# Kernel optimization log

Measured on AMD Instinct MI355X. Metric: run time of the kernel, lower is better.

Reference implementation:

```python
import jax, jax.numpy as jnp
import numpy as np

T, B, IN = 1000, 16, 440
H0, H1 = 512, 512


def setup_inputs() -> dict:
    key = jax.random.key(0)
    ks = iter(jax.random.split(key, 64))

    def w(shape, s=0.02):
        return jax.random.normal(next(ks), shape, jnp.float32) * s

    inp = {"x": jax.random.normal(next(ks), (T, B, IN), jnp.float32)}
    # layer 0 consumes IN features; layer 1 consumes 2*H0 (bidir concat)
    for li, (din, h) in enumerate([(IN, H0), (2 * H0, H1)]):
        for g in "fioc":
            inp[f"W{g}{li}"] = w((h, din))          # x-gate Linear weight
            inp[f"b{g}{li}"] = jnp.zeros((h,), jnp.float32)  # x-gate bias
            inp[f"U{g}{li}"] = w((h, h))            # recurrent Linear (no bias)
    return inp


def _lstm_layer(x, Wf, bf, Wi, bi, Wo, bo, Wc, bc, Uf, Ui, Uo, Uc):
    # Precompute input-to-gate projections for all timesteps (as the torch code does).
    gf = jnp.einsum('tbi,hi->tbh', x, Wf) + bf
    gi = jnp.einsum('tbi,hi->tbh', x, Wi) + bi
    go = jnp.einsum('tbi,hi->tbh', x, Wo) + bo
    gc = jnp.einsum('tbi,hi->tbh', x, Wc) + bc
    B2, H = x.shape[1], Wf.shape[0]

    def step(carry, g):
        ht, ct = carry
        gft, git, got, gct = g
        ft = jax.nn.sigmoid(gft + ht @ Uf.T)
        it = jax.nn.sigmoid(git + ht @ Ui.T)
        ot = jax.nn.sigmoid(got + ht @ Uo.T)
        # drop_mask == 1.0 in eval mode (lstm_drop = 0.0)
        ct = it * jnp.tanh(gct + ht @ Uc.T) + ft * ct
        ht = ot * jnp.tanh(ct)
        return (ht, ct), ht

    init = (jnp.zeros((B2, H), x.dtype), jnp.zeros((B2, H), x.dtype))
    _, h = jax.lax.scan(step, init, (gf, gi, go, gc))
    return h  # [T, B2, H]


def _bidir_layer(x, params):
    Bb = x.shape[1]
    # bidir: concat forward stream with time-flipped stream along batch dim
    x2 = jnp.concatenate([x, x[::-1]], axis=1)
    h = _lstm_layer(x2, *params)
    h_f = h[:, :Bb]
    h_b = h[:, Bb:][::-1]  # flip backward stream back to forward time
    return jnp.concatenate([h_f, h_b], axis=2)


def reference(x,
              Wf0, bf0, Uf0, Wi0, bi0, Ui0, Wo0, bo0, Uo0, Wc0, bc0, Uc0,
              Wf1, bf1, Uf1, Wi1, bi1, Ui1, Wo1, bo1, Uo1, Wc1, bc1, Uc1):
    p0 = (Wf0, bf0, Wi0, bi0, Wo0, bo0, Wc0, bc0, Uf0, Ui0, Uo0, Uc0)
    p1 = (Wf1, bf1, Wi1, bi1, Wo1, bo1, Wc1, bc1, Uf1, Ui1, Uo1, Uc1)
    h = _bidir_layer(x, p0)
    h = _bidir_layer(h, p1)
    return h  # [T, B, 2*H1]
```

## Files before the change

### kernel.cpp

```cpp
#include <hip/hip_runtime.h>
#include <hip/hip_bf16.h>
#include <stdint.h>


typedef __attribute__((ext_vector_type(8))) short bf16x8;
typedef __attribute__((ext_vector_type(4))) float f32x4;
typedef __attribute__((ext_vector_type(4))) int i32x4;

__device__ __forceinline__ unsigned short f2bf(float f) {
    union { float f; unsigned int u; } v; v.f = f;
    unsigned int u = v.u;
    return (unsigned short)((u + 0x7fffu + ((u >> 16) & 1u)) >> 16);
}
__device__ __forceinline__ float bf2f(unsigned short b) {
    union { unsigned int u; float f; } v; v.u = ((unsigned int)b) << 16;
    return v.f;
}
__device__ __forceinline__ float fsig(float x) { return 1.f / (1.f + __expf(-x)); }
__device__ __forceinline__ float ftanh(float x) { return 1.f - 2.f / (1.f + __expf(2.f * x)); }


__device__ __forceinline__ unsigned int coh_ld32(const void* p) {
    unsigned int v;
    asm volatile("global_load_dword %0, %1, off sc0 sc1\n\ts_waitcnt vmcnt(0)"
                 : "=v"(v) : "v"(p) : "memory");
    return v;
}
__device__ __forceinline__ void coh_ld128_issue(i32x4& d, const void* p) {
    asm volatile("global_load_dwordx4 %0, %1, off sc0 sc1" : "=&v"(d) : "v"(p) : "memory");
}
__device__ __forceinline__ void coh_st32(void* p, unsigned int v) {
    asm volatile("global_store_dword %0, %1, off sc0 sc1" :: "v"(p), "v"(v) : "memory");
}
__device__ __forceinline__ void vm_drain() {
    asm volatile("s_waitcnt vmcnt(0)" ::: "memory");
}


__global__ void pack_x_kernel(const float* __restrict__ x, unsigned short* __restrict__ xp,
                              int M, int K, int Kp) {
    int total = M * Kp;
    for (int idx = blockIdx.x * blockDim.x + threadIdx.x; idx < total;
         idx += gridDim.x * blockDim.x) {
        int r = idx / Kp, k = idx - r * Kp;
        xp[idx] = (k < K) ? f2bf(x[(size_t)r * K + k]) : (unsigned short)0;
    }
}

__global__ void pack_w_kernel(const float* __restrict__ Wf, const float* __restrict__ Wi,
                              const float* __restrict__ Wo, const float* __restrict__ Wc,
                              unsigned short* __restrict__ out, int K, int Kp) {
    int total = 2048 * Kp;
    for (int idx = blockIdx.x * blockDim.x + threadIdx.x; idx < total;
         idx += gridDim.x * blockDim.x) {
        int n = idx / Kp, k = idx - n * Kp;
        int gate = n >> 9, j = n & 511;
        const float* W = (gate == 0) ? Wf : (gate == 1) ? Wi : (gate == 2) ? Wo : Wc;
        out[idx] = (k < K) ? f2bf(W[(size_t)j * K + k]) : (unsigned short)0;
    }
}


__global__ __launch_bounds__(256) void gemm_gates(
    const unsigned short* __restrict__ A, const unsigned short* __restrict__ Bm,
    const float* __restrict__ bF, const float* __restrict__ bI,
    const float* __restrict__ bO, const float* __restrict__ bC,
    unsigned short* __restrict__ G, int Kp) {
    __shared__ unsigned short Alds[64][32];
    __shared__ unsigned short Blds[64][32];
    const int tid = threadIdx.x;
    const int m0 = blockIdx.x * 64;
    const int n0 = blockIdx.y * 64;
    const int w = tid >> 6, l = tid & 63;
    const int lr = l & 15, lk = (l >> 4) * 8;
    const int ldrow = tid >> 2;
    const int ldk = (tid & 3) * 8;
    const unsigned short* Aptr = A + (size_t)(m0 + ldrow) * Kp + ldk;
    const unsigned short* Bptr = Bm + (size_t)(n0 + ldrow) * Kp + ldk;

    f32x4 zero = {0.f, 0.f, 0.f, 0.f};
    f32x4 acc0 = zero, acc1 = zero, acc2 = zero, acc3 = zero;

    for (int k0 = 0; k0 < Kp; k0 += 32) {
        *(uint4*)&Alds[ldrow][ldk] = *(const uint4*)(Aptr + k0);
        *(uint4*)&Blds[ldrow][ldk] = *(const uint4*)(Bptr + k0);
        __syncthreads();
        bf16x8 a = *(const bf16x8*)&Alds[w * 16 + lr][lk];
        bf16x8 b0 = *(const bf16x8*)&Blds[0 * 16 + lr][lk];
        bf16x8 b1 = *(const bf16x8*)&Blds[1 * 16 + lr][lk];
        bf16x8 b2 = *(const bf16x8*)&Blds[2 * 16 + lr][lk];
        bf16x8 b3 = *(const bf16x8*)&Blds[3 * 16 + lr][lk];
        acc0 = __builtin_amdgcn_mfma_f32_16x16x32_bf16(a, b0, acc0, 0, 0, 0);
        acc1 = __builtin_amdgcn_mfma_f32_16x16x32_bf16(a, b1, acc1, 0, 0, 0);
        acc2 = __builtin_amdgcn_mfma_f32_16x16x32_bf16(a, b2, acc2, 0, 0, 0);
        acc3 = __builtin_amdgcn_mfma_f32_16x16x32_bf16(a, b3, acc3, 0, 0, 0);
        __syncthreads();
    }
    const int gate = n0 >> 9;
    const float* bias = (gate == 0) ? bF : (gate == 1) ? bI : (gate == 2) ? bO : bC;
    f32x4 accs[4] = {acc0, acc1, acc2, acc3};
#pragma unroll
    for (int c = 0; c < 4; ++c) {
        int col = n0 + c * 16 + lr;
        float bv = bias[col & 511];
#pragma unroll
        for (int r = 0; r < 4; ++r) {
            int row = m0 + w * 16 + (l >> 4) * 4 + r;
            G[(size_t)row * 2048 + col] = f2bf(accs[c][r] + bv);
        }
    }
}


template <int LAYER>
__global__ __launch_bounds__(256, 1) void lstm_rec4(
    const unsigned short* __restrict__ U, const unsigned short* __restrict__ G,
    unsigned short* __restrict__ y_bf, float* __restrict__ y_f32,
    unsigned short* __restrict__ h_frag, unsigned int* __restrict__ flags, int T) {
    __shared__ unsigned short wlds[4 * 16 * 64 * 8];

    const int tid = threadIdx.x;
    const int w = tid >> 6;
    const int l = tid & 63;
    const int wg = blockIdx.x;
    const int j0 = wg * 16;
    const int g = l & 3;
    const int q = (l & 15) >> 2;
    const int jl = 4 * w + q;
    const int m0 = (l >> 4) * 4 + g;
    const int mrow = (l >> 4) * 4;
    const int colg = g * 512 + j0 + jl;
    const int kcw = wg >> 1;
    const int jlq = ((wg & 1) << 4) + jl;
    const int lslot = m0 + 16 * (jlq >> 3);
    const int jb = jlq & 7;

    for (int e = tid; e < 4096; e += 256) {
        int fl = e >> 6;
        int ll = e & 63;
        int nt = fl >> 4, kc = fl & 15;
        int nl = nt * 16 + (ll & 15);
        int jj = nl >> 2, gg = nl & 3;
        int nglob = gg * 512 + j0 + jj;
        int k = kc * 32 + (ll >> 4) * 8;
        *(uint4*)&wlds[(size_t)e * 8] = *(const uint4*)&U[(size_t)nglob * 512 + k];
    }

    {
        unsigned int* h0w = (unsigned int*)h_frag;
        coh_st32(&h0w[wg * 256 + tid], 0u);
        vm_drain();
        __syncthreads();
        if (tid == 0) coh_st32(&flags[wg * 32], 1u);
    }

    unsigned short gpf[2][4];
    {
        const unsigned short* gf_ = G + (size_t)mrow * 2048 + colg;
        const unsigned short* gb_ = G + (size_t)((T - 1) * 16 + mrow) * 2048 + colg;
#pragma unroll
        for (int r = 0; r < 4; ++r) {
            gpf[0][r] = gf_[r * 2048];
            gpf[1][r] = gb_[r * 2048];
        }
    }

    float cst[2][4] = {{0.f, 0.f, 0.f, 0.f}, {0.f, 0.f, 0.f, 0.f}};

    for (int s = 0; s < T; ++s) {
        unsigned short gcur[2][4];
#pragma unroll
        for (int r = 0; r < 4; ++r) {
            gcur[0][r] = gpf[0][r];
            gcur[1][r] = gpf[1][r];
        }
        {
            int sn = (s + 1 < T) ? (s + 1) : (T - 1);
            const unsigned short* gf_ = G + (size_t)(sn * 16 + mrow) * 2048 + colg;
            const unsigned short* gb_ = G + (size_t)((T - 1 - sn) * 16 + mrow) * 2048 + colg;
#pragma unroll
            for (int r = 0; r < 4; ++r) {
                gpf[0][r] = gf_[r * 2048];
                gpf[1][r] = gb_[r * 2048];
            }
        }

        if (w == 0) {
            unsigned tgt = (unsigned)(s + 1);
            int guard = 0;
            while (true) {
                unsigned u = 0xFFFFFFFFu;
                if (l < 32) u = coh_ld32(&flags[l * 32]);
                if (__all(u >= tgt) || ++guard > (1 << 14)) break;
            }
        }
        __syncthreads();

        const unsigned short* hb = h_frag + (size_t)(s & 1) * 16384;
        i32x4 ha0[16], ha1[16];
#pragma unroll
        for (int kc = 0; kc < 16; ++kc) {
            coh_ld128_issue(ha0[kc], hb + ((size_t)(0 * 16 + kc) * 64 + l) * 8);
            coh_ld128_issue(ha1[kc], hb + ((size_t)(1 * 16 + kc) * 64 + l) * 8);
        }
        vm_drain();
        __builtin_amdgcn_sched_barrier(0);

        f32x4 acc0 = {0.f, 0.f, 0.f, 0.f};
        f32x4 acc1 = {0.f, 0.f, 0.f, 0.f};
#pragma unroll
        for (int kc = 0; kc < 16; ++kc) {
            union { i32x4 i; bf16x8 v; } c0, c1;
            c0.i = ha0[kc];
            c1.i = ha1[kc];
            bf16x8 bw = *(const bf16x8*)&wlds[(((size_t)w * 16 + kc) * 64 + l) * 8];
            acc0 = __builtin_amdgcn_mfma_f32_16x16x32_bf16(c0.v, bw, acc0, 0, 0, 0);
            acc1 = __builtin_amdgcn_mfma_f32_16x16x32_bf16(c1.v, bw, acc1, 0, 0, 0);
        }

        float hsel[2];
#pragma unroll
        for (int mb = 0; mb < 2; ++mb) {
            f32x4 acc = mb ? acc1 : acc0;
#pragma unroll
            for (int r = 0; r < 4; ++r) {
                float v = acc[r] + bf2f(gcur[mb][r]);
                float x1 = __shfl_xor(v, 1, 64);
                float x2 = __shfl_xor(v, 2, 64);
                float x3 = __shfl_xor(x1, 2, 64);
                bool b0 = (g & 1) != 0, b1 = (g & 2) != 0;
                float gf = b1 ? (b0 ? x3 : x2) : (b0 ? x1 : v);
                float gi = b1 ? (b0 ? x2 : x3) : (b0 ? v : x1);
                float go = b1 ? (b0 ? x1 : v) : (b0 ? x3 : x2);
                float gc = b1 ? (b0 ? v : x1) : (b0 ? x2 : x3);
                float ft = fsig(gf), it = fsig(gi), ot = fsig(go);
                float cn = it * ftanh(gc) + ft * cst[mb][r];
                cst[mb][r] = cn;
                float hn = ot * ftanh(cn);
                if (r == g) hsel[mb] = hn;
            }
        }

        const int p1 = (s + 1) & 1;
        unsigned hw0, hw1;
        float ho0, ho1;
        {
            unsigned b16 = (unsigned)f2bf(hsel[0]);
            unsigned ho = (unsigned)__shfl_xor((int)b16, 4, 64);
            hw0 = b16 | (ho << 16);
            ho0 = __shfl_xor(hsel[0], 4, 64);
            b16 = (unsigned)f2bf(hsel[1]);
            ho = (unsigned)__shfl_xor((int)b16, 4, 64);
            hw1 = b16 | (ho << 16);
            ho1 = __shfl_xor(hsel[1], 4, 64);
        }
        if ((q & 1) == 0) {
#pragma unroll
            for (int mb = 0; mb < 2; ++mb) {
                unsigned word = mb ? hw1 : hw0;
                size_t base =
                    (size_t)p1 * 16384 + ((size_t)(mb * 16 + kcw) * 64 + lslot) * 8 + jb;
                coh_st32(h_frag + base, word);
                int row = (mb ? (T - 1 - s) : s) * 16 + m0;
                int col = mb * 512 + j0 + jl;
                if (LAYER == 0) {
                    *(unsigned int*)&y_bf[(size_t)row * 1024 + col] = word;
                } else {
                    float2 fv = make_float2(hsel[mb], mb ? ho1 : ho0);
                    *(float2*)&y_f32[(size_t)row * 1024 + col] = fv;
                }
            }
        }

        vm_drain();
        __syncthreads();
        if (tid == 0) coh_st32(&flags[wg * 32], (unsigned)(s + 2));
    }
}


extern "C" void kernel_launch(void* const* d_in, const int* in_sizes, int n_in,
                              void* d_out, int out_size, void* d_ws, size_t ws_size,
                              hipStream_t stream) {
    (void)in_sizes; (void)n_in; (void)out_size; (void)ws_size;
    const int T = 1000, M = T * 16;
    const int K0 = 440, K0p = 448, K1 = 1024;

    char* ws = (char*)d_ws;
    size_t off = 0;
    auto alloc = [&](size_t bytes) -> void* {
        void* p = ws + off;
        off += (bytes + 255) & ~(size_t)255;
        return p;
    };
    unsigned short* G  = (unsigned short*)alloc((size_t)M * 2048 * 2);
    unsigned short* xp = (unsigned short*)alloc((size_t)M * K0p * 2);
    unsigned short* W0 = (unsigned short*)alloc((size_t)2048 * K0p * 2);
    unsigned short* W1 = (unsigned short*)alloc((size_t)2048 * K1 * 2);
    unsigned short* U0 = (unsigned short*)alloc((size_t)2048 * 512 * 2);
    unsigned short* U1 = (unsigned short*)alloc((size_t)2048 * 512 * 2);
    unsigned short* y0 = (unsigned short*)alloc((size_t)M * 1024 * 2);
    unsigned short* hf = (unsigned short*)alloc((size_t)2 * 16384 * 2);
    unsigned int* fl0  = (unsigned int*)alloc((size_t)32 * 32 * 4);
    unsigned int* fl1  = (unsigned int*)alloc((size_t)32 * 32 * 4);

    const float* x = (const float*)d_in[0];

    hipMemsetAsync(fl0, 0, 32 * 32 * 4, stream);
    hipMemsetAsync(fl1, 0, 32 * 32 * 4, stream);

    pack_x_kernel<<<2048, 256, 0, stream>>>(x, xp, M, K0, K0p);
    pack_w_kernel<<<1024, 256, 0, stream>>>((const float*)d_in[1], (const float*)d_in[4],
                                            (const float*)d_in[7], (const float*)d_in[10],
                                            W0, K0, K0p);
    pack_w_kernel<<<1024, 256, 0, stream>>>((const float*)d_in[3], (const float*)d_in[6],
                                            (const float*)d_in[9], (const float*)d_in[12],
                                            U0, 512, 512);
    pack_w_kernel<<<1024, 256, 0, stream>>>((const float*)d_in[13], (const float*)d_in[16],
                                            (const float*)d_in[19], (const float*)d_in[22],
                                            W1, K1, K1);
    pack_w_kernel<<<1024, 256, 0, stream>>>((const float*)d_in[15], (const float*)d_in[18],
                                            (const float*)d_in[21], (const float*)d_in[24],
                                            U1, 512, 512);

    dim3 blk(256);
    dim3 g0(M / 64, 2048 / 64);
    gemm_gates<<<g0, blk, 0, stream>>>(xp, W0, (const float*)d_in[2], (const float*)d_in[5],
                                       (const float*)d_in[8], (const float*)d_in[11], G, K0p);
    lstm_rec4<0><<<32, 256, 0, stream>>>(U0, G, y0, nullptr, hf, fl0, T);
    gemm_gates<<<g0, blk, 0, stream>>>(y0, W1, (const float*)d_in[14], (const float*)d_in[17],
                                       (const float*)d_in[20], (const float*)d_in[23], G, K1);
    lstm_rec4<1><<<32, 256, 0, stream>>>(U1, G, nullptr, (float*)d_out, hf, fl1, T);
}
```

Before: 9.566 ms.

## Replace flag barrier with per-word step tags on hidden state exchange

Drops the per-block flag counters and the spin-wait followed by a separate hidden-state load. Each hidden value is now stored as a 32-bit word that carries the step number in its upper half, and consumers poll the whole tagged buffer until every tag matches. The untagged values are staged in LDS for the MFMA. This removes a serial round trip (flag poll, then data load) and the drain-plus-barrier before each flag store, at the cost of doubling the exchanged bytes and re-reading the full buffer on every failed poll.

Measured after the change: 11.24 ms. 1.18x slower.

```diff
diff --git a/kernel.cpp b/kernel.cpp
--- a/kernel.cpp
+++ b/kernel.cpp
@@ -20,16 +20,10 @@
 __device__ __forceinline__ float ftanh(float x) { return 1.f - 2.f / (1.f + __expf(2.f * x)); }
 
 
-__device__ __forceinline__ unsigned int coh_ld32(const void* p) {
-    unsigned int v;
-    asm volatile("global_load_dword %0, %1, off sc0 sc1\n\ts_waitcnt vmcnt(0)"
-                 : "=v"(v) : "v"(p) : "memory");
-    return v;
-}
-__device__ __forceinline__ void coh_ld128_issue(i32x4& d, const void* p) {
+__device__ __forceinline__ void mall_ld128_issue(i32x4& d, const void* p) {
     asm volatile("global_load_dwordx4 %0, %1, off sc0 sc1" : "=&v"(d) : "v"(p) : "memory");
 }
-__device__ __forceinline__ void coh_st32(void* p, unsigned int v) {
+__device__ __forceinline__ void mall_st32(void* p, unsigned int v) {
     asm volatile("global_store_dword %0, %1, off sc0 sc1" :: "v"(p), "v"(v) : "memory");
 }
 __device__ __forceinline__ void vm_drain() {
@@ -113,11 +107,13 @@
 
 
 template <int LAYER>
-__global__ __launch_bounds__(256, 1) void lstm_rec4(
+__global__ __launch_bounds__(256, 1) void lstm_rec6(
     const unsigned short* __restrict__ U, const unsigned short* __restrict__ G,
     unsigned short* __restrict__ y_bf, float* __restrict__ y_f32,
-    unsigned short* __restrict__ h_frag, unsigned int* __restrict__ flags, int T) {
+    unsigned int* __restrict__ tg, int T) {
     __shared__ unsigned short wlds[4 * 16 * 64 * 8];
+    __shared__ unsigned short hstage[2 * 16 * 64 * 8];
+    __shared__ int sh_ok[8];
 
     const int tid = threadIdx.x;
     const int w = tid >> 6;
@@ -134,6 +130,8 @@
     const int jlq = ((wg & 1) << 4) + jl;
     const int lslot = m0 + 16 * (jlq >> 3);
     const int jb = jlq & 7;
+    const int fidx0 = ((0 * 16 + kcw) * 64 + lslot) * 8 + jb;
+    const int fidx1 = ((1 * 16 + kcw) * 64 + lslot) * 8 + jb;
 
     for (int e = tid; e < 4096; e += 256) {
         int fl = e >> 6;
@@ -145,14 +143,7 @@
         int k = kc * 32 + (ll >> 4) * 8;
         *(uint4*)&wlds[(size_t)e * 8] = *(const uint4*)&U[(size_t)nglob * 512 + k];
     }
-
-    {
-        unsigned int* h0w = (unsigned int*)h_frag;
-        coh_st32(&h0w[wg * 256 + tid], 0u);
-        vm_drain();
-        __syncthreads();
-        if (tid == 0) coh_st32(&flags[wg * 32], 1u);
-    }
+    __syncthreads();
 
     unsigned short gpf[2][4];
     {
@@ -185,38 +176,50 @@
             }
         }
 
-        if (w == 0) {
-            unsigned tgt = (unsigned)(s + 1);
-            int guard = 0;
-            while (true) {
-                unsigned u = 0xFFFFFFFFu;
-                if (l < 32) u = coh_ld32(&flags[l * 32]);
-                if (__all(u >= tgt) || ++guard > (1 << 14)) break;
-            }
-        }
-        __syncthreads();
-
-        const unsigned short* hb = h_frag + (size_t)(s & 1) * 16384;
-        i32x4 ha0[16], ha1[16];
-#pragma unroll
-        for (int kc = 0; kc < 16; ++kc) {
-            coh_ld128_issue(ha0[kc], hb + ((size_t)(0 * 16 + kc) * 64 + l) * 8);
-            coh_ld128_issue(ha1[kc], hb + ((size_t)(1 * 16 + kc) * 64 + l) * 8);
-        }
-        vm_drain();
-        __builtin_amdgcn_sched_barrier(0);
-
         f32x4 acc0 = {0.f, 0.f, 0.f, 0.f};
         f32x4 acc1 = {0.f, 0.f, 0.f, 0.f};
-#pragma unroll
-        for (int kc = 0; kc < 16; ++kc) {
-            union { i32x4 i; bf16x8 v; } c0, c1;
-            c0.i = ha0[kc];
-            c1.i = ha1[kc];
-            bf16x8 bw = *(const bf16x8*)&wlds[(((size_t)w * 16 + kc) * 64 + l) * 8];
-            acc0 = __builtin_amdgcn_mfma_f32_16x16x32_bf16(c0.v, bw, acc0, 0, 0, 0);
-            acc1 = __builtin_amdgcn_mfma_f32_16x16x32_bf16(c1.v, bw, acc1, 0, 0, 0);
-        }
+
+        if (s > 0) {
+            const uint4* tg4 = (const uint4*)(tg + (size_t)(s & 1) * 16384);
+            const unsigned tagw = (unsigned)s << 16;
+            int attempt = 0;
+            for (;;) {
+                i32x4 v[16];
+#pragma unroll
+                for (int i = 0; i < 16; ++i)
+                    mall_ld128_issue(v[i], tg4 + (tid + 256 * i));
+                vm_drain();
+                __builtin_amdgcn_sched_barrier(0);
+                bool ok = true;
+#pragma unroll
+                for (int i = 0; i < 16; ++i) {
+                    unsigned a = (unsigned)v[i][0], b = (unsigned)v[i][1];
+                    unsigned c = (unsigned)v[i][2], d = (unsigned)v[i][3];
+                    ok &= ((a & 0xffff0000u) == tagw) & ((b & 0xffff0000u) == tagw) &
+                          ((c & 0xffff0000u) == tagw) & ((d & 0xffff0000u) == tagw);
+                    uint2 pk;
+                    pk.x = (a & 0xffffu) | (b << 16);
+                    pk.y = (c & 0xffffu) | (d << 16);
+                    ((uint2*)hstage)[tid + 256 * i] = pk;
+                }
+                bool wok = __all((int)ok);
+                if (l == 0) sh_ok[(attempt & 1) * 4 + w] = wok ? 1 : 0;
+                __syncthreads();
+                int sl = (attempt & 1) * 4;
+                if (sh_ok[sl + 0] & sh_ok[sl + 1] & sh_ok[sl + 2] & sh_ok[sl + 3]) break;
+                if (++attempt > (1 << 11)) break;
+            }
+
+#pragma unroll
+            for (int kc = 0; kc < 16; ++kc) {
+                bf16x8 a0 = *(const bf16x8*)&hstage[((size_t)(0 * 16 + kc) * 64 + l) * 8];
+                bf16x8 a1 = *(const bf16x8*)&hstage[((size_t)(1 * 16 + kc) * 64 + l) * 8];
+                bf16x8 bw = *(const bf16x8*)&wlds[(((size_t)w * 16 + kc) * 64 + l) * 8];
+                acc0 = __builtin_amdgcn_mfma_f32_16x16x32_bf16(a0, bw, acc0, 0, 0, 0);
+                acc1 = __builtin_amdgcn_mfma_f32_16x16x32_bf16(a1, bw, acc1, 0, 0, 0);
+            }
+        }
+        __syncthreads();
 
         float hsel[2];
 #pragma unroll
@@ -241,7 +244,13 @@
             }
         }
 
-        const int p1 = (s + 1) & 1;
+        {
+            const unsigned tagn = (unsigned)(s + 1) << 16;
+            unsigned int* tgw = tg + (size_t)((s + 1) & 1) * 16384;
+            mall_st32(&tgw[fidx0], tagn | (unsigned)f2bf(hsel[0]));
+            mall_st32(&tgw[fidx1], tagn | (unsigned)f2bf(hsel[1]));
+        }
+
         unsigned hw0, hw1;
         float ho0, ho1;
         {
@@ -257,24 +266,16 @@
         if ((q & 1) == 0) {
 #pragma unroll
             for (int mb = 0; mb < 2; ++mb) {
-                unsigned word = mb ? hw1 : hw0;
-                size_t base =
-                    (size_t)p1 * 16384 + ((size_t)(mb * 16 + kcw) * 64 + lslot) * 8 + jb;
-                coh_st32(h_frag + base, word);
                 int row = (mb ? (T - 1 - s) : s) * 16 + m0;
                 int col = mb * 512 + j0 + jl;
                 if (LAYER == 0) {
-                    *(unsigned int*)&y_bf[(size_t)row * 1024 + col] = word;
+                    *(unsigned int*)&y_bf[(size_t)row * 1024 + col] = mb ? hw1 : hw0;
                 } else {
                     float2 fv = make_float2(hsel[mb], mb ? ho1 : ho0);
                     *(float2*)&y_f32[(size_t)row * 1024 + col] = fv;
                 }
             }
         }
-
-        vm_drain();
-        __syncthreads();
-        if (tid == 0) coh_st32(&flags[wg * 32], (unsigned)(s + 2));
     }
 }
 
@@ -300,14 +301,13 @@
     unsigned short* U0 = (unsigned short*)alloc((size_t)2048 * 512 * 2);
     unsigned short* U1 = (unsigned short*)alloc((size_t)2048 * 512 * 2);
     unsigned short* y0 = (unsigned short*)alloc((size_t)M * 1024 * 2);
-    unsigned short* hf = (unsigned short*)alloc((size_t)2 * 16384 * 2);
-    unsigned int* fl0  = (unsigned int*)alloc((size_t)32 * 32 * 4);
-    unsigned int* fl1  = (unsigned int*)alloc((size_t)32 * 32 * 4);
+    unsigned int* tg0  = (unsigned int*)alloc((size_t)2 * 16384 * 4);
+    unsigned int* tg1  = (unsigned int*)alloc((size_t)2 * 16384 * 4);
 
     const float* x = (const float*)d_in[0];
 
-    hipMemsetAsync(fl0, 0, 32 * 32 * 4, stream);
-    hipMemsetAsync(fl1, 0, 32 * 32 * 4, stream);
+    hipMemsetAsync(tg0, 0, (size_t)2 * 16384 * 4, stream);
+    hipMemsetAsync(tg1, 0, (size_t)2 * 16384 * 4, stream);
 
     pack_x_kernel<<<2048, 256, 0, stream>>>(x, xp, M, K0, K0p);
     pack_w_kernel<<<1024, 256, 0, stream>>>((const float*)d_in[1], (const float*)d_in[4],
@@ -327,8 +327,8 @@
     dim3 g0(M / 64, 2048 / 64);
     gemm_gates<<<g0, blk, 0, stream>>>(xp, W0, (const float*)d_in[2], (const float*)d_in[5],
                                        (const float*)d_in[8], (const float*)d_in[11], G, K0p);
-    lstm_rec4<0><<<32, 256, 0, stream>>>(U0, G, y0, nullptr, hf, fl0, T);
+    lstm_rec6<0><<<32, 256, 0, stream>>>(U0, G, y0, nullptr, tg0, T);
     gemm_gates<<<g0, blk, 0, stream>>>(y0, W1, (const float*)d_in[14], (const float*)d_in[17],
                                        (const float*)d_in[20], (const float*)d_in[23], G, K1);
-    lstm_rec4<1><<<32, 256, 0, stream>>>(U1, G, nullptr, (float*)d_out, hf, fl1, T);
-}
+    lstm_rec6<1><<<32, 256, 0, stream>>>(U1, G, nullptr, (float*)d_out, tg1, T);
+}
```

## Use per-wave flags and LDS-staged hidden state in persistent LSTM recurrence

Applied to the files above, without the earlier changes.

Replaces the per-workgroup step flag with a flag per wave, so each wave publishes its hidden-state slice as soon as its own stores drain, with no block-wide barrier first. Each wave now loads only a quarter of the shared hidden vector from global memory into a double-buffered LDS stage. After one barrier all waves read their MFMA operands from LDS instead of every wave issuing 32 coherent global loads. It also skips the recurrent matmul at step zero instead of zero-initialising h, moves the gate prefetch and output stores after the flag publish, and gives each layer its own h buffer. The trade-off is polling 128 flags instead of 32 and extra LDS traffic.

After: 8.869 ms. -7.3%, faster.

```diff
diff --git a/kernel.cpp b/kernel.cpp
--- a/kernel.cpp
+++ b/kernel.cpp
@@ -113,11 +113,12 @@
 
 
 template <int LAYER>
-__global__ __launch_bounds__(256, 1) void lstm_rec4(
+__global__ __launch_bounds__(256, 1) void lstm_rec9(
     const unsigned short* __restrict__ U, const unsigned short* __restrict__ G,
     unsigned short* __restrict__ y_bf, float* __restrict__ y_f32,
-    unsigned short* __restrict__ h_frag, unsigned int* __restrict__ flags, int T) {
+    unsigned int* __restrict__ h_frag, unsigned int* __restrict__ flags, int T) {
     __shared__ unsigned short wlds[4 * 16 * 64 * 8];
+    __shared__ unsigned short hstage[2][16 * 64 * 8 * 2];
 
     const int tid = threadIdx.x;
     const int w = tid >> 6;
@@ -134,6 +135,9 @@
     const int jlq = ((wg & 1) << 4) + jl;
     const int lslot = m0 + 16 * (jlq >> 3);
     const int jb = jlq & 7;
+    const int fid0 = (0 * 16 + kcw) * 256 + lslot * 4 + (jb >> 1);
+    const int fid1 = (1 * 16 + kcw) * 256 + lslot * 4 + (jb >> 1);
+    unsigned int* const flagp = flags + (size_t)(wg * 4 + w) * 32;
 
     for (int e = tid; e < 4096; e += 256) {
         int fl = e >> 6;
@@ -146,14 +150,6 @@
         *(uint4*)&wlds[(size_t)e * 8] = *(const uint4*)&U[(size_t)nglob * 512 + k];
     }
 
-    {
-        unsigned int* h0w = (unsigned int*)h_frag;
-        coh_st32(&h0w[wg * 256 + tid], 0u);
-        vm_drain();
-        __syncthreads();
-        if (tid == 0) coh_st32(&flags[wg * 32], 1u);
-    }
-
     unsigned short gpf[2][4];
     {
         const unsigned short* gf_ = G + (size_t)mrow * 2048 + colg;
@@ -168,54 +164,49 @@
     float cst[2][4] = {{0.f, 0.f, 0.f, 0.f}, {0.f, 0.f, 0.f, 0.f}};
 
     for (int s = 0; s < T; ++s) {
-        unsigned short gcur[2][4];
-#pragma unroll
-        for (int r = 0; r < 4; ++r) {
-            gcur[0][r] = gpf[0][r];
-            gcur[1][r] = gpf[1][r];
-        }
-        {
-            int sn = (s + 1 < T) ? (s + 1) : (T - 1);
-            const unsigned short* gf_ = G + (size_t)(sn * 16 + mrow) * 2048 + colg;
-            const unsigned short* gb_ = G + (size_t)((T - 1 - sn) * 16 + mrow) * 2048 + colg;
-#pragma unroll
-            for (int r = 0; r < 4; ++r) {
-                gpf[0][r] = gf_[r * 2048];
-                gpf[1][r] = gb_[r * 2048];
-            }
-        }
-
-        if (w == 0) {
-            unsigned tgt = (unsigned)(s + 1);
-            int guard = 0;
-            while (true) {
-                unsigned u = 0xFFFFFFFFu;
-                if (l < 32) u = coh_ld32(&flags[l * 32]);
-                if (__all(u >= tgt) || ++guard > (1 << 14)) break;
+        if (s > 0) {
+            {
+                const unsigned tgt = (unsigned)(s + 1);
+                const unsigned int* fp = flags + (size_t)(32 * w + (l & 31)) * 32;
+                int guard = 0;
+                for (;;) {
+                    unsigned u = 0xFFFFFFFFu;
+                    if (l < 32) u = coh_ld32(fp);
+                    if (__all(u >= tgt) || ++guard > (1 << 14)) break;
+                }
+            }
+            {
+                const unsigned int* src = h_frag + (size_t)(s & 1) * 8192;
+                unsigned int* dst = (unsigned int*)hstage[s & 1];
+                const int half = (l >> 5);
+                i32x4 v[8];
+                int gd[8];
+#pragma unroll
+                for (int i = 0; i < 8; ++i) {
+                    int strip = half * 32 + 8 * w + i;
+                    gd[i] = strip * 128 + (l & 31) * 4;
+                    coh_ld128_issue(v[i], src + gd[i]);
+                }
+                vm_drain();
+                __builtin_amdgcn_sched_barrier(0);
+#pragma unroll
+                for (int i = 0; i < 8; ++i) *(i32x4*)(dst + gd[i]) = v[i];
             }
         }
         __syncthreads();
-
-        const unsigned short* hb = h_frag + (size_t)(s & 1) * 16384;
-        i32x4 ha0[16], ha1[16];
-#pragma unroll
-        for (int kc = 0; kc < 16; ++kc) {
-            coh_ld128_issue(ha0[kc], hb + ((size_t)(0 * 16 + kc) * 64 + l) * 8);
-            coh_ld128_issue(ha1[kc], hb + ((size_t)(1 * 16 + kc) * 64 + l) * 8);
-        }
-        vm_drain();
-        __builtin_amdgcn_sched_barrier(0);
 
         f32x4 acc0 = {0.f, 0.f, 0.f, 0.f};
         f32x4 acc1 = {0.f, 0.f, 0.f, 0.f};
-#pragma unroll
-        for (int kc = 0; kc < 16; ++kc) {
-            union { i32x4 i; bf16x8 v; } c0, c1;
-            c0.i = ha0[kc];
-            c1.i = ha1[kc];
-            bf16x8 bw = *(const bf16x8*)&wlds[(((size_t)w * 16 + kc) * 64 + l) * 8];
-            acc0 = __builtin_amdgcn_mfma_f32_16x16x32_bf16(c0.v, bw, acc0, 0, 0, 0);
-            acc1 = __builtin_amdgcn_mfma_f32_16x16x32_bf16(c1.v, bw, acc1, 0, 0, 0);
+        if (s > 0) {
+            const unsigned short* hs = hstage[s & 1];
+#pragma unroll
+            for (int kc = 0; kc < 16; ++kc) {
+                bf16x8 a0 = *(const bf16x8*)&hs[((size_t)(0 * 16 + kc) * 64 + l) * 8];
+                bf16x8 a1 = *(const bf16x8*)&hs[((size_t)(1 * 16 + kc) * 64 + l) * 8];
+                bf16x8 bw = *(const bf16x8*)&wlds[(((size_t)w * 16 + kc) * 64 + l) * 8];
+                acc0 = __builtin_amdgcn_mfma_f32_16x16x32_bf16(a0, bw, acc0, 0, 0, 0);
+                acc1 = __builtin_amdgcn_mfma_f32_16x16x32_bf16(a1, bw, acc1, 0, 0, 0);
+            }
         }
 
         float hsel[2];
@@ -224,7 +215,7 @@
             f32x4 acc = mb ? acc1 : acc0;
 #pragma unroll
             for (int r = 0; r < 4; ++r) {
-                float v = acc[r] + bf2f(gcur[mb][r]);
+                float v = acc[r] + bf2f(gpf[mb][r]);
                 float x1 = __shfl_xor(v, 1, 64);
                 float x2 = __shfl_xor(v, 2, 64);
                 float x3 = __shfl_xor(x1, 2, 64);
@@ -241,7 +232,6 @@
             }
         }
 
-        const int p1 = (s + 1) & 1;
         unsigned hw0, hw1;
         float ho0, ho1;
         {
@@ -254,27 +244,40 @@
             hw1 = b16 | (ho << 16);
             ho1 = __shfl_xor(hsel[1], 4, 64);
         }
+
+        {
+            unsigned int* hfw = h_frag + (size_t)((s + 1) & 1) * 8192;
+            if ((q & 1) == 0) {
+                coh_st32(hfw + fid0, hw0);
+                coh_st32(hfw + fid1, hw1);
+            }
+            vm_drain();
+            if (l == 0) coh_st32(flagp, (unsigned)(s + 2));
+        }
+
+        {
+            int sn = (s + 1 < T) ? (s + 1) : (T - 1);
+            const unsigned short* gf_ = G + (size_t)(sn * 16 + mrow) * 2048 + colg;
+            const unsigned short* gb_ = G + (size_t)((T - 1 - sn) * 16 + mrow) * 2048 + colg;
+#pragma unroll
+            for (int r = 0; r < 4; ++r) {
+                gpf[0][r] = gf_[r * 2048];
+                gpf[1][r] = gb_[r * 2048];
+            }
+        }
         if ((q & 1) == 0) {
 #pragma unroll
             for (int mb = 0; mb < 2; ++mb) {
-                unsigned word = mb ? hw1 : hw0;
-                size_t base =
-                    (size_t)p1 * 16384 + ((size_t)(mb * 16 + kcw) * 64 + lslot) * 8 + jb;
-                coh_st32(h_frag + base, word);
                 int row = (mb ? (T - 1 - s) : s) * 16 + m0;
                 int col = mb * 512 + j0 + jl;
                 if (LAYER == 0) {
-                    *(unsigned int*)&y_bf[(size_t)row * 1024 + col] = word;
+                    *(unsigned int*)&y_bf[(size_t)row * 1024 + col] = mb ? hw1 : hw0;
                 } else {
                     float2 fv = make_float2(hsel[mb], mb ? ho1 : ho0);
                     *(float2*)&y_f32[(size_t)row * 1024 + col] = fv;
                 }
             }
         }
-
-        vm_drain();
-        __syncthreads();
-        if (tid == 0) coh_st32(&flags[wg * 32], (unsigned)(s + 2));
     }
 }
 
@@ -300,14 +303,15 @@
     unsigned short* U0 = (unsigned short*)alloc((size_t)2048 * 512 * 2);
     unsigned short* U1 = (unsigned short*)alloc((size_t)2048 * 512 * 2);
     unsigned short* y0 = (unsigned short*)alloc((size_t)M * 1024 * 2);
-    unsigned short* hf = (unsigned short*)alloc((size_t)2 * 16384 * 2);
-    unsigned int* fl0  = (unsigned int*)alloc((size_t)32 * 32 * 4);
-    unsigned int* fl1  = (unsigned int*)alloc((size_t)32 * 32 * 4);
+    unsigned int* hf0  = (unsigned int*)alloc((size_t)2 * 8192 * 4);
+    unsigned int* hf1  = (unsigned int*)alloc((size_t)2 * 8192 * 4);
+    unsigned int* fl0  = (unsigned int*)alloc((size_t)128 * 32 * 4);
+    unsigned int* fl1  = (unsigned int*)alloc((size_t)128 * 32 * 4);
 
     const float* x = (const float*)d_in[0];
 
-    hipMemsetAsync(fl0, 0, 32 * 32 * 4, stream);
-    hipMemsetAsync(fl1, 0, 32 * 32 * 4, stream);
+    hipMemsetAsync(fl0, 0, 128 * 32 * 4, stream);
+    hipMemsetAsync(fl1, 0, 128 * 32 * 4, stream);
 
     pack_x_kernel<<<2048, 256, 0, stream>>>(x, xp, M, K0, K0p);
     pack_w_kernel<<<1024, 256, 0, stream>>>((const float*)d_in[1], (const float*)d_in[4],
@@ -327,8 +331,8 @@
     dim3 g0(M / 64, 2048 / 64);
     gemm_gates<<<g0, blk, 0, stream>>>(xp, W0, (const float*)d_in[2], (const float*)d_in[5],
                                        (const float*)d_in[8], (const float*)d_in[11], G, K0p);
-    lstm_rec4<0><<<32, 256, 0, stream>>>(U0, G, y0, nullptr, hf, fl0, T);
+    lstm_rec9<0><<<32, 256, 0, stream>>>(U0, G, y0, nullptr, hf0, fl0, T);
     gemm_gates<<<g0, blk, 0, stream>>>(y0, W1, (const float*)d_in[14], (const float*)d_in[17],
                                        (const float*)d_in[20], (const float*)d_in[23], G, K1);
-    lstm_rec4<1><<<32, 256, 0, stream>>>(U1, G, nullptr, (float*)d_out, hf, fl1, T);
-}
+    lstm_rec9<1><<<32, 256, 0, stream>>>(U1, G, nullptr, (float*)d_out, hf1, fl1, T);
+}
```
